# Performance work log

Measured on AMD Instinct MI355X. Metric: run time of the kernel, lower is better.

## Reference

```python
import jax, jax.numpy as jnp
import numpy as np


def setup_inputs() -> dict:
    key = jax.random.key(0)
    k1, k2 = jax.random.split(key)
    B, C, H, W = 2, 1, 64, 64
    HW = H * W
    pred = jax.random.uniform(k1, (B, C, H, W), dtype=jnp.float32)
    token = jax.random.uniform(k2, (B, HW, HW), dtype=jnp.float32)
    return {"pred": pred, "token": token}


def reference(pred, token):
    # pred: [B, 1, H, W] -> p: [B, HW]
    B = pred.shape[0]
    p = pred.reshape(B, -1)
    q = 1.0 - p
    # sum(f_token)  = sum_bij p_bi * token_bij
    # sum(fore_A)   = sum_bij p_bi * token_bij * p_bj  (bilinear quadratic form)
    # sum(b_token)  = sum_bij (1-p_bi) * token_bij
    # sum(back_B)   = sum_bij (1-p_bi) * token_bij * (1-p_bj)
    s_f = jnp.einsum('bi,bij->', p, token)
    s_fa = jnp.einsum('bi,bij,bj->', p, token, p)
    s_b = jnp.einsum('bi,bij->', q, token)
    s_bb = jnp.einsum('bi,bij,bj->', q, token, q)
    gsa_loss = 2.0 - s_fa / s_f - s_bb / s_b
    return gsa_loss
```

## Files before the change

kernel.cpp:

```cpp
#include <hip/hip_runtime.h>


#define HW   4096
#define HW4  1024
#define NBLK 2048

struct alignas(32) D4 { double t, f, c, fa; };

__global__ __launch_bounds__(256, 4) void gsa_partial(
    const float* __restrict__ pred,
    const float* __restrict__ token,
    D4* __restrict__ part)
{
    __shared__ float4 pj_lds[HW4];
    __shared__ double sm[4][4];

    const float4* __restrict__ tok4  = (const float4*)token;
    const float4* __restrict__ pred4 = (const float4*)pred;

    const int bid  = blockIdx.x;
    const int b    = bid >> 10;
    const int wave = threadIdx.x >> 6;
    const int lane = threadIdx.x & 63;
    const int row  = bid * 4 + wave;

    const float4* __restrict__ rowp = tok4 + (size_t)row * HW4;

    float4 t[16];
#pragma unroll
    for (int u = 0; u < 16; ++u)
        t[u] = rowp[u * 64 + lane];

    __builtin_amdgcn_sched_barrier(0);

    for (int k = threadIdx.x; k < HW4; k += 256)
        pj_lds[k] = pred4[b * HW4 + k];
    const float pi = pred[row];

    __syncthreads();

    float s0 = 0.f, s1 = 0.f, d0 = 0.f, d1 = 0.f;
#pragma unroll
    for (int u = 0; u < 16; u += 2) {
        float4 pa = pj_lds[u * 64 + lane];
        float4 pb = pj_lds[(u + 1) * 64 + lane];
        s0 += t[u].x + t[u].y + t[u].z + t[u].w;
        d0 += t[u].x * pa.x + t[u].y * pa.y + t[u].z * pa.z + t[u].w * pa.w;
        s1 += t[u+1].x + t[u+1].y + t[u+1].z + t[u+1].w;
        d1 += t[u+1].x * pb.x + t[u+1].y * pb.y + t[u+1].z * pb.z + t[u+1].w * pb.w;
    }
    float s = s0 + s1, d = d0 + d1;

    float tT  = s;
    float tF  = pi * s;
    float tC  = d;
    float tFA = pi * d;

    for (int off = 32; off > 0; off >>= 1) {
        tT  += __shfl_down(tT,  off);
        tF  += __shfl_down(tF,  off);
        tC  += __shfl_down(tC,  off);
        tFA += __shfl_down(tFA, off);
    }

    if (lane == 0) {
        sm[wave][0] = (double)tT;
        sm[wave][1] = (double)tF;
        sm[wave][2] = (double)tC;
        sm[wave][3] = (double)tFA;
    }
    __syncthreads();

    if (threadIdx.x == 0) {
        D4 p;
        p.t  = sm[0][0] + sm[1][0] + sm[2][0] + sm[3][0];
        p.f  = sm[0][1] + sm[1][1] + sm[2][1] + sm[3][1];
        p.c  = sm[0][2] + sm[1][2] + sm[2][2] + sm[3][2];
        p.fa = sm[0][3] + sm[1][3] + sm[2][3] + sm[3][3];
        part[bid] = p;
    }
}

__global__ __launch_bounds__(256) void gsa_final(
    const D4* __restrict__ part, float* __restrict__ out)
{
    const double2* __restrict__ p2 = (const double2*)part;

    double aT = 0.0, aF = 0.0, aC = 0.0, aFA = 0.0;
    for (int k = threadIdx.x; k < NBLK; k += 256) {
        double2 lo = p2[k * 2 + 0];
        double2 hi = p2[k * 2 + 1];
        aT += lo.x; aF += lo.y; aC += hi.x; aFA += hi.y;
    }

    for (int off = 32; off > 0; off >>= 1) {
        aT  += __shfl_down(aT,  off);
        aF  += __shfl_down(aF,  off);
        aC  += __shfl_down(aC,  off);
        aFA += __shfl_down(aFA, off);
    }

    __shared__ double sm[4][4];
    const int wave = threadIdx.x >> 6;
    const int lane = threadIdx.x & 63;
    if (lane == 0) {
        sm[wave][0] = aT; sm[wave][1] = aF;
        sm[wave][2] = aC; sm[wave][3] = aFA;
    }
    __syncthreads();

    if (threadIdx.x == 0) {
        double T   = sm[0][0] + sm[1][0] + sm[2][0] + sm[3][0];
        double sf  = sm[0][1] + sm[1][1] + sm[2][1] + sm[3][1];
        double sc  = sm[0][2] + sm[1][2] + sm[2][2] + sm[3][2];
        double sfa = sm[0][3] + sm[1][3] + sm[2][3] + sm[3][3];
        double sb  = T - sf;
        double sbb = T - sf - sc + sfa;
        out[0] = (float)(2.0 - sfa / sf - sbb / sb);
    }
}

extern "C" void kernel_launch(void* const* d_in, const int* in_sizes, int n_in,
                              void* d_out, int out_size, void* d_ws, size_t ws_size,
                              hipStream_t stream)
{
    const float* pred  = (const float*)d_in[0];
    const float* token = (const float*)d_in[1];
    float* out  = (float*)d_out;
    D4*    part = (D4*)d_ws;

    gsa_partial<<<NBLK, 256, 0, stream>>>(pred, token, part);
    gsa_final<<<1, 256, 0, stream>>>(part, out);
}
```

Before: 29.92 us.

## Process four rows per wave with double-buffered register prefetch

Each wave now handles four token rows instead of one, so the grid drops from 2048 to 512 blocks. The pred vector is loaded into LDS once per block and reused across more rows, and the partial-result array that the final kernel must reduce shrinks. While one row is being reduced, the next row is loaded into a second register buffer to overlap memory with compute. In exchange, register use roughly doubles (launch bounds lowered to 2 blocks per SM) and there are fewer blocks to hide latency on a memory-bound 32MB stream.

New measurement: 30.09 us. Within noise of the previous version (+0.6%).

```diff
diff --git a/kernel.cpp b/kernel.cpp
--- a/kernel.cpp
+++ b/kernel.cpp
@@ -3,11 +3,12 @@
 
 #define HW   4096
 #define HW4  1024
-#define NBLK 2048
+#define NBLK 512
+#define RPW  4
 
 struct alignas(32) D4 { double t, f, c, fa; };
 
-__global__ __launch_bounds__(256, 4) void gsa_partial(
+__global__ __launch_bounds__(256, 2) void gsa_partial(
     const float* __restrict__ pred,
     const float* __restrict__ token,
     D4* __restrict__ part)
@@ -19,42 +20,62 @@
     const float4* __restrict__ pred4 = (const float4*)pred;
 
     const int bid  = blockIdx.x;
-    const int b    = bid >> 10;
     const int wave = threadIdx.x >> 6;
     const int lane = threadIdx.x & 63;
-    const int row  = bid * 4 + wave;
-
-    const float4* __restrict__ rowp = tok4 + (size_t)row * HW4;
-
-    float4 t[16];
-#pragma unroll
-    for (int u = 0; u < 16; ++u)
-        t[u] = rowp[u * 64 + lane];
-
-    __builtin_amdgcn_sched_barrier(0);
+    const int gw   = bid * 4 + wave;
+    const int row0 = gw * RPW;
+    const int b    = row0 >> 12;
 
     for (int k = threadIdx.x; k < HW4; k += 256)
         pj_lds[k] = pred4[b * HW4 + k];
-    const float pi = pred[row];
+
+    float pi_r[RPW];
+#pragma unroll
+    for (int r = 0; r < RPW; ++r)
+        pi_r[r] = pred[row0 + r];
+
+    float4 A[16], Bv[16];
+    {
+        const float4* __restrict__ rp = tok4 + (size_t)row0 * HW4;
+#pragma unroll
+        for (int u = 0; u < 16; ++u)
+            A[u] = rp[u * 64 + lane];
+    }
 
     __syncthreads();
 
-    float s0 = 0.f, s1 = 0.f, d0 = 0.f, d1 = 0.f;
+    float tT = 0.f, tF = 0.f, tC = 0.f, tFA = 0.f;
+
 #pragma unroll
-    for (int u = 0; u < 16; u += 2) {
-        float4 pa = pj_lds[u * 64 + lane];
-        float4 pb = pj_lds[(u + 1) * 64 + lane];
-        s0 += t[u].x + t[u].y + t[u].z + t[u].w;
-        d0 += t[u].x * pa.x + t[u].y * pa.y + t[u].z * pa.z + t[u].w * pa.w;
-        s1 += t[u+1].x + t[u+1].y + t[u+1].z + t[u+1].w;
-        d1 += t[u+1].x * pb.x + t[u+1].y * pb.y + t[u+1].z * pb.z + t[u+1].w * pb.w;
+    for (int r = 0; r < RPW; ++r) {
+        float4* cur = (r & 1) ? Bv : A;
+        float4* nxt = (r & 1) ? A  : Bv;
+
+        if (r + 1 < RPW) {
+            const float4* __restrict__ rp = tok4 + (size_t)(row0 + r + 1) * HW4;
+#pragma unroll
+            for (int u = 0; u < 16; ++u)
+                nxt[u] = rp[u * 64 + lane];
+        }
+        __builtin_amdgcn_sched_barrier(0);
+
+        float s0 = 0.f, s1 = 0.f, d0 = 0.f, d1 = 0.f;
+#pragma unroll
+        for (int u = 0; u < 16; u += 2) {
+            float4 pa = pj_lds[u * 64 + lane];
+            float4 pb = pj_lds[(u + 1) * 64 + lane];
+            s0 += cur[u].x + cur[u].y + cur[u].z + cur[u].w;
+            d0 += cur[u].x * pa.x + cur[u].y * pa.y + cur[u].z * pa.z + cur[u].w * pa.w;
+            s1 += cur[u+1].x + cur[u+1].y + cur[u+1].z + cur[u+1].w;
+            d1 += cur[u+1].x * pb.x + cur[u+1].y * pb.y + cur[u+1].z * pb.z + cur[u+1].w * pb.w;
+        }
+        float s = s0 + s1, d = d0 + d1;
+        float pi = pi_r[r];
+        tT  += s;
+        tF  += pi * s;
+        tC  += d;
+        tFA += pi * d;
     }
-    float s = s0 + s1, d = d0 + d1;
-
-    float tT  = s;
-    float tF  = pi * s;
-    float tC  = d;
-    float tFA = pi * d;
 
     for (int off = 32; off > 0; off >>= 1) {
         tT  += __shfl_down(tT,  off);
```
